# Optimization experiments

Measured on AMD Instinct MI355X. Metric: run time of the kernel, lower is better.

## Reference

```python
import jax, jax.numpy as jnp
import numpy as np
import math

N_HEAD = 16

def _rope_cos_sin(T, head_dim):
    # thetas[i] = 10000 ** (-2*(i-1)/dim) for i = 1..dim/2  ->  exponent -2*j/dim, j=0..dim/2-1
    j = jnp.arange(head_dim // 2, dtype=jnp.float32)
    theta = jnp.power(10000.0, -2.0 * j / head_dim)          # [d/2]
    t = jnp.arange(T, dtype=jnp.float32)                      # [T]
    ang = t[:, None] * theta[None, :]                         # [T, d/2]
    return jnp.cos(ang), jnp.sin(ang)

def _apply_rope(u, cos, sin):
    # u: [B,H,T,d]; interleaved complex rotation over pairs (u[...,2i], u[...,2i+1])
    B, H, T, d = u.shape
    u = u.reshape(B, H, T, d // 2, 2)
    u0, u1 = u[..., 0], u[..., 1]
    r0 = u0 * cos - u1 * sin
    r1 = u0 * sin + u1 * cos
    return jnp.stack([r0, r1], axis=-1).reshape(B, H, T, d)

def setup_inputs() -> dict:
    key = jax.random.key(0)
    ks = jax.random.split(key, 9)
    C = 1024
    s = 1.0 / math.sqrt(C)
    return {
        "x": jax.random.normal(ks[0], (4, 2048, C), dtype=jnp.float32),
        "wq": jax.random.normal(ks[1], (C, C), dtype=jnp.float32) * s,
        "bq": jax.random.normal(ks[2], (C,), dtype=jnp.float32) * s,
        "wk": jax.random.normal(ks[3], (C, C), dtype=jnp.float32) * s,
        "bk": jax.random.normal(ks[4], (C,), dtype=jnp.float32) * s,
        "wv": jax.random.normal(ks[5], (C, C), dtype=jnp.float32) * s,
        "bv": jax.random.normal(ks[6], (C,), dtype=jnp.float32) * s,
        "wp": jax.random.normal(ks[7], (C, C), dtype=jnp.float32) * s,
        "bp": jax.random.normal(ks[8], (C,), dtype=jnp.float32) * s,
    }

def reference(x, wq, bq, wk, bk, wv, bv, wp, bp):
    B, T, C = x.shape
    H = N_HEAD
    d = C // H
    def proj(w, b):
        # nn.Linear: x @ w.T + b, then split heads -> [B,H,T,d]
        return (jnp.einsum('btc,oc->bto', x, w) + b).reshape(B, T, H, d).transpose(0, 2, 1, 3)
    q, k, v = proj(wq, bq), proj(wk, bk), proj(wv, bv)
    cos, sin = _rope_cos_sin(T, d)
    q = _apply_rope(q, cos, sin)
    k = _apply_rope(k, cos, sin)
    att = jnp.einsum('bhqd,bhkd->bhqk', q, k) * (1.0 / math.sqrt(d))  # [B,H,T,T]
    causal = jnp.tril(jnp.ones((T, T), dtype=bool))
    att = jnp.where(causal, att, jnp.finfo(att.dtype).min)
    att = jax.nn.softmax(att, axis=-1)
    y = jnp.einsum('bhqk,bhkd->bhqd', att, v)                         # [B,H,T,d]
    y = y.transpose(0, 2, 1, 3).reshape(B, T, C)
    return jnp.einsum('btc,oc->bto', y, wp) + bp
```

## Files before the change

### kernel.cpp

```cpp
#include <hip/hip_runtime.h>

typedef __attribute__((ext_vector_type(8))) __bf16 bf16x8;
typedef __attribute__((ext_vector_type(4))) float f32x4;
typedef __attribute__((ext_vector_type(16))) float f32x16;
typedef unsigned short u16;

#define TSEQ   2048
#define NB     4
#define NHEAD  16
#define HDIM   64
#define CMODEL 1024
#define MTOK   (NB*TSEQ)

__device__ __forceinline__ u16 f2bf(float x){
  unsigned u = __float_as_uint(x);
  u += 0x7fffu + ((u >> 16) & 1u);
  return (u16)(u >> 16);
}

__device__ __forceinline__ unsigned cvtpk(float lo, float hi){
  unsigned r;
  asm("v_cvt_pk_bf16_f32 %0, %1, %2" : "=v"(r) : "v"(lo), "v"(hi));
  return r;
}
__device__ __forceinline__ void plswap(unsigned &a, unsigned &b){
  asm volatile("v_permlane32_swap_b32 %0, %1" : "+v"(a), "+v"(b));
}

__device__ __forceinline__ void async16(const void* g, const u16* lds_base){
  __builtin_amdgcn_global_load_lds(
      (const __attribute__((address_space(1))) unsigned*)(uintptr_t)g,
      (__attribute__((address_space(3))) unsigned*)(unsigned)(uintptr_t)lds_base,
      16, 0, 0);
}

__global__ void cast_bf16_kernel(const float* __restrict__ src, u16* __restrict__ dst, int n4){
  int i = blockIdx.x * blockDim.x + threadIdx.x;
  int stride = gridDim.x * blockDim.x;
  for (; i < n4; i += stride){
    float4 v = ((const float4*)src)[i];
    ((ushort4*)dst)[i] = make_ushort4(f2bf(v.x), f2bf(v.y), f2bf(v.z), f2bf(v.w));
  }
}

__global__ void cast4_bf16_kernel(const float* __restrict__ s0, const float* __restrict__ s1,
                                  const float* __restrict__ s2, const float* __restrict__ s3,
                                  u16* __restrict__ d0, u16* __restrict__ d1,
                                  u16* __restrict__ d2, u16* __restrict__ d3, int n4){
  int which = blockIdx.y;
  const float* s = (which==0)?s0:(which==1)?s1:(which==2)?s2:s3;
  u16* d        = (which==0)?d0:(which==1)?d1:(which==2)?d2:d3;
  int i = blockIdx.x * blockDim.x + threadIdx.x;
  int stride = gridDim.x * blockDim.x;
  for (; i < n4; i += stride){
    float4 v = ((const float4*)s)[i];
    ((ushort4*)d)[i] = make_ushort4(f2bf(v.x), f2bf(v.y), f2bf(v.z), f2bf(v.w));
  }
}

__global__ void rope_table_kernel(float2* __restrict__ rope){
  int i = blockIdx.x * blockDim.x + threadIdx.x;
  if (i >= TSEQ * (HDIM/2)) return;
  int t = i >> 5, j = i & 31;
  float theta = exp2f(-(float)j * (13.287712379549449f / 32.f));
  float ang = (float)t * theta;
  rope[i] = make_float2(cosf(ang), sinf(ang));
}

#define AREG 8192
#define BREG 16384

__device__ __forceinline__ void gemm_tb3_mainloop(
    const u16* __restrict__ A, const u16* __restrict__ B,
    int m0, int n0, u16* sAb, u16* sBb, f32x4 acc[4][4])
{
  const int tid = threadIdx.x;
  const int lane = tid & 63, w = tid >> 6;
  const int ln = lane & 15, g = lane >> 4;
  const int wm = w >> 2, wn = w & 3;

  const f32x4 zero = {0.f, 0.f, 0.f, 0.f};
#pragma unroll
  for (int i = 0; i < 4; ++i)
#pragma unroll
    for (int nt = 0; nt < 4; ++nt) acc[i][nt] = zero;

  const int cA0 = tid,       rA0 = cA0 >> 3;
  const int cA1 = 512 + tid, rA1 = cA1 >> 3;
  const u16* aS0 = A + (size_t)(m0 + rA0)*CMODEL + (((cA0 & 7) ^ (rA0 & 7)) << 3);
  const u16* aS1 = A + (size_t)(m0 + rA1)*CMODEL + (((cA1 & 7) ^ (rA1 & 7)) << 3);
  const unsigned dA0 = (unsigned)cA0 * 8, dA1 = (unsigned)cA1 * 8;
  const u16* bS[4]; unsigned dB[4];
#pragma unroll
  for (int j = 0; j < 4; ++j){
    int c = j*512 + tid, r = c >> 3;
    bS[j] = B + (size_t)(n0 + r)*CMODEL + (((c & 7) ^ (r & 7)) << 3);
    dB[j] = (unsigned)c * 8;
  }

  unsigned aoff[4][2], boff[4][2];
#pragma unroll
  for (int i = 0; i < 4; ++i){
    int r = wm*64 + i*16 + ln;
#pragma unroll
    for (int kk = 0; kk < 2; ++kk)
      aoff[i][kk] = (unsigned)(r*8 + ((kk*4 + g) ^ (r & 7))) * 8;
  }
#pragma unroll
  for (int nt = 0; nt < 4; ++nt){
    int r = wn*64 + nt*16 + ln;
#pragma unroll
    for (int kk = 0; kk < 2; ++kk)
      boff[nt][kk] = (unsigned)(r*8 + ((kk*4 + g) ^ (r & 7))) * 8;
  }

  async16(aS0,       sAb + dA0);
  async16(aS1,       sAb + dA1);
  async16(bS[0],     sBb + dB[0]);
  async16(bS[1],     sBb + dB[1]);
  async16(bS[2],     sBb + dB[2]);
  async16(bS[3],     sBb + dB[3]);
  async16(aS0 + 64,  sAb + AREG + dA0);
  async16(aS1 + 64,  sAb + AREG + dA1);
  async16(bS[0] + 64, sBb + BREG + dB[0]);
  async16(bS[1] + 64, sBb + BREG + dB[1]);
  async16(bS[2] + 64, sBb + BREG + dB[2]);
  async16(bS[3] + 64, sBb + BREG + dB[3]);
  asm volatile("s_waitcnt vmcnt(6)" ::: "memory");
  asm volatile("s_barrier" ::: "memory");

#pragma unroll 1
  for (int kt = 0; kt < 16; ++kt){
    const int cb = kt % 3;
    const int nb = (kt + 2) % 3;
    const u16* Ab = sAb + cb*AREG;
    const u16* Bb = sBb + cb*BREG;
    u16* An = sAb + nb*AREG;
    u16* Bn = sBb + nb*BREG;
    const unsigned ko = (unsigned)(kt + 2) * 64u;
    const bool st = (kt < 14);

    bf16x8 a0, a1, a2, a3, b0, b1, b2, b3;

    a0 = *(const bf16x8*)&Ab[aoff[0][0]];
    a1 = *(const bf16x8*)&Ab[aoff[1][0]];
    b0 = *(const bf16x8*)&Bb[boff[0][0]];
    b1 = *(const bf16x8*)&Bb[boff[1][0]];
    b2 = *(const bf16x8*)&Bb[boff[2][0]];
    b3 = *(const bf16x8*)&Bb[boff[3][0]];
    if (st){ async16(aS0 + ko, An + dA0); async16(aS1 + ko, An + dA1); }
    asm volatile("s_barrier" ::: "memory");
    __builtin_amdgcn_s_setprio(1);
    acc[0][0] = __builtin_amdgcn_mfma_f32_16x16x32_bf16(a0, b0, acc[0][0], 0,0,0);
    acc[0][1] = __builtin_amdgcn_mfma_f32_16x16x32_bf16(a0, b1, acc[0][1], 0,0,0);
    acc[0][2] = __builtin_amdgcn_mfma_f32_16x16x32_bf16(a0, b2, acc[0][2], 0,0,0);
    acc[0][3] = __builtin_amdgcn_mfma_f32_16x16x32_bf16(a0, b3, acc[0][3], 0,0,0);
    acc[1][0] = __builtin_amdgcn_mfma_f32_16x16x32_bf16(a1, b0, acc[1][0], 0,0,0);
    acc[1][1] = __builtin_amdgcn_mfma_f32_16x16x32_bf16(a1, b1, acc[1][1], 0,0,0);
    acc[1][2] = __builtin_amdgcn_mfma_f32_16x16x32_bf16(a1, b2, acc[1][2], 0,0,0);
    acc[1][3] = __builtin_amdgcn_mfma_f32_16x16x32_bf16(a1, b3, acc[1][3], 0,0,0);
    __builtin_amdgcn_s_setprio(0);
    asm volatile("s_barrier" ::: "memory");

    a2 = *(const bf16x8*)&Ab[aoff[2][0]];
    a3 = *(const bf16x8*)&Ab[aoff[3][0]];
    if (st){ async16(bS[0] + ko, Bn + dB[0]); async16(bS[1] + ko, Bn + dB[1]); }
    asm volatile("s_barrier" ::: "memory");
    __builtin_amdgcn_s_setprio(1);
    acc[2][0] = __builtin_amdgcn_mfma_f32_16x16x32_bf16(a2, b0, acc[2][0], 0,0,0);
    acc[2][1] = __builtin_amdgcn_mfma_f32_16x16x32_bf16(a2, b1, acc[2][1], 0,0,0);
    acc[2][2] = __builtin_amdgcn_mfma_f32_16x16x32_bf16(a2, b2, acc[2][2], 0,0,0);
    acc[2][3] = __builtin_amdgcn_mfma_f32_16x16x32_bf16(a2, b3, acc[2][3], 0,0,0);
    acc[3][0] = __builtin_amdgcn_mfma_f32_16x16x32_bf16(a3, b0, acc[3][0], 0,0,0);
    acc[3][1] = __builtin_amdgcn_mfma_f32_16x16x32_bf16(a3, b1, acc[3][1], 0,0,0);
    acc[3][2] = __builtin_amdgcn_mfma_f32_16x16x32_bf16(a3, b2, acc[3][2], 0,0,0);
    acc[3][3] = __builtin_amdgcn_mfma_f32_16x16x32_bf16(a3, b3, acc[3][3], 0,0,0);
    __builtin_amdgcn_s_setprio(0);
    asm volatile("s_barrier" ::: "memory");

    a0 = *(const bf16x8*)&Ab[aoff[0][1]];
    a1 = *(const bf16x8*)&Ab[aoff[1][1]];
    b0 = *(const bf16x8*)&Bb[boff[0][1]];
    b1 = *(const bf16x8*)&Bb[boff[1][1]];
    b2 = *(const bf16x8*)&Bb[boff[2][1]];
    b3 = *(const bf16x8*)&Bb[boff[3][1]];
    if (st) async16(bS[2] + ko, Bn + dB[2]);
    asm volatile("s_barrier" ::: "memory");
    __builtin_amdgcn_s_setprio(1);
    acc[0][0] = __builtin_amdgcn_mfma_f32_16x16x32_bf16(a0, b0, acc[0][0], 0,0,0);
    acc[0][1] = __builtin_amdgcn_mfma_f32_16x16x32_bf16(a0, b1, acc[0][1], 0,0,0);
    acc[0][2] = __builtin_amdgcn_mfma_f32_16x16x32_bf16(a0, b2, acc[0][2], 0,0,0);
    acc[0][3] = __builtin_amdgcn_mfma_f32_16x16x32_bf16(a0, b3, acc[0][3], 0,0,0);
    acc[1][0] = __builtin_amdgcn_mfma_f32_16x16x32_bf16(a1, b0, acc[1][0], 0,0,0);
    acc[1][1] = __builtin_amdgcn_mfma_f32_16x16x32_bf16(a1, b1, acc[1][1], 0,0,0);
    acc[1][2] = __builtin_amdgcn_mfma_f32_16x16x32_bf16(a1, b2, acc[1][2], 0,0,0);
    acc[1][3] = __builtin_amdgcn_mfma_f32_16x16x32_bf16(a1, b3, acc[1][3], 0,0,0);
    __builtin_amdgcn_s_setprio(0);
    asm volatile("s_barrier" ::: "memory");

    a2 = *(const bf16x8*)&Ab[aoff[2][1]];
    a3 = *(const bf16x8*)&Ab[aoff[3][1]];
    if (st) async16(bS[3] + ko, Bn + dB[3]);
    asm volatile("s_barrier" ::: "memory");
    __builtin_amdgcn_s_setprio(1);
    acc[2][0] = __builtin_amdgcn_mfma_f32_16x16x32_bf16(a2, b0, acc[2][0], 0,0,0);
    acc[2][1] = __builtin_amdgcn_mfma_f32_16x16x32_bf16(a2, b1, acc[2][1], 0,0,0);
    acc[2][2] = __builtin_amdgcn_mfma_f32_16x16x32_bf16(a2, b2, acc[2][2], 0,0,0);
    acc[2][3] = __builtin_amdgcn_mfma_f32_16x16x32_bf16(a2, b3, acc[2][3], 0,0,0);
    acc[3][0] = __builtin_amdgcn_mfma_f32_16x16x32_bf16(a3, b0, acc[3][0], 0,0,0);
    acc[3][1] = __builtin_amdgcn_mfma_f32_16x16x32_bf16(a3, b1, acc[3][1], 0,0,0);
    acc[3][2] = __builtin_amdgcn_mfma_f32_16x16x32_bf16(a3, b2, acc[3][2], 0,0,0);
    acc[3][3] = __builtin_amdgcn_mfma_f32_16x16x32_bf16(a3, b3, acc[3][3], 0,0,0);
    __builtin_amdgcn_s_setprio(0);
    if (st) asm volatile("s_waitcnt vmcnt(6)" ::: "memory");
    else    asm volatile("s_waitcnt vmcnt(0)" ::: "memory");
    asm volatile("s_barrier" ::: "memory");
  }
}

#define SCQ 0.18033688011112042f

__global__ __launch_bounds__(512, 1) void gemm_qkv_kernel(
    const u16* __restrict__ xb,
    const u16* __restrict__ wqb, const u16* __restrict__ wkb, const u16* __restrict__ wvb,
    const float* __restrict__ bq, const float* __restrict__ bk, const float* __restrict__ bv,
    const float2* __restrict__ rope,
    u16* __restrict__ Qh, u16* __restrict__ Kh, u16* __restrict__ Vt)
{
  __shared__ u16 sA[3*AREG];
  __shared__ u16 sB[3*BREG];
  const int z = blockIdx.z;
  const u16*  W    = (z == 0) ? wqb : (z == 1) ? wkb : wvb;
  const float* bias = (z == 0) ? bq  : (z == 1) ? bk  : bv;
  const int m0 = blockIdx.y * 128, n0 = blockIdx.x * 256;

  f32x4 acc[4][4];
  gemm_tb3_mainloop(xb, W, m0, n0, sA, sB, acc);

  const int tid = threadIdx.x, w = tid >> 6, lane = tid & 63;
  const int ln = lane & 15, g = lane >> 4;
  const int wm = w >> 2, wn = w & 3;

#pragma unroll
  for (int mt = 0; mt < 4; ++mt){
#pragma unroll
    for (int nt = 0; nt < 4; ++nt){
      int o  = n0 + wn*64 + nt*16 + ln;
      float bb = bias[o];
      int h  = o >> 6;
      int dd = o & 63;
      if (z < 2){
        int j = dd >> 1;
        u16* dst = (z == 0) ? Qh : Kh;
        float qs = (z == 0) ? SCQ : 1.0f;
#pragma unroll
        for (int rr = 0; rr < 4; ++rr){
          int t  = m0 + wm*64 + mt*16 + g*4 + rr;
          int b  = t >> 11, tt = t & (TSEQ-1);
          float v  = acc[mt][nt][rr] + bb;
          float pv = __shfl_xor(v, 1);
          float2 cs = rope[tt*32 + j];
          float out = ((o & 1) == 0) ? (v*cs.x - pv*cs.y) : (pv*cs.y + v*cs.x);
          dst[(size_t)((b*NHEAD + h)*TSEQ + tt)*HDIM + dd] = f2bf(out * qs);
        }
      } else {
        int t0 = m0 + wm*64 + mt*16 + g*4;
        int b  = t0 >> 11, tt0 = t0 & (TSEQ-1);
        u16 pk[4];
#pragma unroll
        for (int rr = 0; rr < 4; ++rr) pk[rr] = f2bf(acc[mt][nt][rr] + bb);
        *(ushort4*)&Vt[(size_t)((b*NHEAD + h)*HDIM + dd)*TSEQ + tt0] =
            make_ushort4(pk[0], pk[1], pk[2], pk[3]);
      }
    }
  }
}

__global__ __launch_bounds__(128) void attn_kernel(
    const u16* __restrict__ Qh, const u16* __restrict__ Kh,
    const u16* __restrict__ Vt, u16* __restrict__ yb)
{
  __shared__ u16 sK[2][64*64];
  __shared__ u16 sV[2][64*64];

  const int tid = threadIdx.x, w = tid >> 6, lane = tid & 63;
  const int ln = lane & 31, hi = lane >> 5;

  const int bid = blockIdx.x;
  const int t   = 31 - (bid >> 6);
  const int bh  = (bid & 7) * 8 + ((bid >> 3) & 7);
  const int b   = bh >> 4, h = bh & (NHEAD-1);

  const u16* Qbase = Qh + (size_t)bh * TSEQ * HDIM;
  const u16* Kbase = Kh + (size_t)bh * TSEQ * HDIM;
  const u16* Vbase = Vt + (size_t)bh * HDIM * TSEQ;

  const int r0 = t*64 + w*32;

  const int swz = ln & 7;
  const f32x16 zero16 = {0,0,0,0,0,0,0,0,0,0,0,0,0,0,0,0};

  const u16* kp[4]; const u16* vp[4]; unsigned dstc[4];
#pragma unroll
  for (int i = 0; i < 4; ++i){
    int c = i*128 + tid, r = c >> 3, pc = c & 7;
    kp[i]   = Kbase + (size_t)r*HDIM + ((pc ^ (r&7))<<3);
    vp[i]   = Vbase + (size_t)r*TSEQ + ((pc ^ (r&7))<<3);
    dstc[i] = (unsigned)(i*128 + w*64)*8;
  }

  unsigned offd[4];
#pragma unroll
  for (int d = 0; d < 4; ++d) offd[d] = ((unsigned)((2*d + hi) ^ swz)) * 8;
  const unsigned rowl = (unsigned)ln * 64;
  const unsigned rowh = rowl + 32*64;

  bf16x8 qf[4];
#pragma unroll
  for (int ds = 0; ds < 4; ++ds)
    qf[ds] = *(const bf16x8*)&Qbase[(size_t)(r0 + ln)*HDIM + ds*16 + hi*8];

  f32x16 yacc0 = zero16, yacc1 = zero16;
  float m2 = -1e30f, lp = 0.f;

  int buf = 0;
#pragma unroll
  for (int i = 0; i < 4; ++i){
    async16(kp[i], sK[0] + dstc[i]);
    async16(vp[i], sV[0] + dstc[i]);
  }

#pragma unroll 1
  for (int jt = 0; jt <= t; ++jt){
    __syncthreads();
    if (jt < t){
      const size_t ko = (size_t)(jt+1) * (64*HDIM);
      const size_t vo = (size_t)(jt+1) * 64;
      u16* sKb = sK[buf^1]; u16* sVb = sV[buf^1];
#pragma unroll
      for (int i = 0; i < 4; ++i){
        async16(kp[i] + ko, sKb + dstc[i]);
        async16(vp[i] + vo, sVb + dstc[i]);
      }
    }

    const u16* sKb = sK[buf];
    const u16* sVb = sV[buf];
    const bool full1 = (jt < t) || w;

    f32x16 p0 = zero16, p1 = zero16;
    __builtin_amdgcn_s_setprio(1);
#pragma unroll
    for (int ds = 0; ds < 4; ++ds){
      bf16x8 k0 = *(const bf16x8*)&sKb[rowl + offd[ds]];
      p0 = __builtin_amdgcn_mfma_f32_32x32x16_bf16(k0, qf[ds], p0, 0, 0, 0);
    }
    if (full1){
#pragma unroll
      for (int ds = 0; ds < 4; ++ds){
        bf16x8 k1 = *(const bf16x8*)&sKb[rowh + offd[ds]];
        p1 = __builtin_amdgcn_mfma_f32_32x32x16_bf16(k1, qf[ds], p1, 0, 0, 0);
      }
    }
    __builtin_amdgcn_s_setprio(0);

    if (jt == t){
#pragma unroll
      for (int r = 0; r < 16; ++r){
        int k0r = (r&3) + 8*(r>>2) + 4*hi;
        bool cut = k0r > ln;
        if (!w){ if (cut) p0[r] = -1e30f; }
        else   { if (cut) p1[r] = -1e30f; }
      }
    }

    float lm = p0[0];
#pragma unroll
    for (int r = 1; r < 16; ++r) lm = fmaxf(lm, p0[r]);
    if (full1){
#pragma unroll
      for (int r = 0; r < 16; ++r) lm = fmaxf(lm, p1[r]);
    }

    if (__any(lm - m2 > 8.0f)){
      float lmp = __shfl_xor(lm, 32);
      float mn  = fmaxf(m2, fmaxf(lm, lmp));
      float scl = exp2f(m2 - mn);
      m2 = mn;
      lp *= scl;
#pragma unroll
      for (int r = 0; r < 16; ++r){
        float sr = __shfl(scl, (r&3) + 8*(r>>2) + 4*hi);
        yacc0[r] *= sr; yacc1[r] *= sr;
      }
    }

    float ts = 0.f;
#pragma unroll
    for (int r = 0; r < 16; ++r){ p0[r] = exp2f(p0[r] - m2); ts += p0[r]; }
    if (full1){
#pragma unroll
      for (int r = 0; r < 16; ++r){ p1[r] = exp2f(p1[r] - m2); ts += p1[r]; }
    }
    lp += ts;

    bf16x8 pa[4];
    {
      union { unsigned u[4]; bf16x8 v; } f0, f1;
      unsigned A0 = cvtpk(p0[0], p0[1]),  B0 = cvtpk(p0[2], p0[3]);
      unsigned A1 = cvtpk(p0[4], p0[5]),  B1 = cvtpk(p0[6], p0[7]);
      plswap(A0, A1); plswap(B0, B1);
      f0.u[0]=A0; f0.u[1]=B0; f0.u[2]=A1; f0.u[3]=B1;  pa[0]=f0.v;
      unsigned A2 = cvtpk(p0[8], p0[9]),  B2 = cvtpk(p0[10], p0[11]);
      unsigned A3 = cvtpk(p0[12], p0[13]),B3 = cvtpk(p0[14], p0[15]);
      plswap(A2, A3); plswap(B2, B3);
      f1.u[0]=A2; f1.u[1]=B2; f1.u[2]=A3; f1.u[3]=B3;  pa[1]=f1.v;
    }
    if (full1){
      union { unsigned u[4]; bf16x8 v; } f2, f3;
      unsigned A4 = cvtpk(p1[0], p1[1]),  B4 = cvtpk(p1[2], p1[3]);
      unsigned A5 = cvtpk(p1[4], p1[5]),  B5 = cvtpk(p1[6], p1[7]);
      plswap(A4, A5); plswap(B4, B5);
      f2.u[0]=A4; f2.u[1]=B4; f2.u[2]=A5; f2.u[3]=B5;  pa[2]=f2.v;
      unsigned A6 = cvtpk(p1[8], p1[9]),  B6 = cvtpk(p1[10], p1[11]);
      unsigned A7 = cvtpk(p1[12], p1[13]),B7 = cvtpk(p1[14], p1[15]);
      plswap(A6, A7); plswap(B6, B7);
      f3.u[0]=A6; f3.u[1]=B6; f3.u[2]=A7; f3.u[3]=B7;  pa[3]=f3.v;
    }

    __builtin_amdgcn_s_setprio(1);
#pragma unroll
    for (int st = 0; st < 2; ++st){
      bf16x8 v0 = *(const bf16x8*)&sVb[rowl + offd[st]];
      bf16x8 v1 = *(const bf16x8*)&sVb[rowh + offd[st]];
      yacc0 = __builtin_amdgcn_mfma_f32_32x32x16_bf16(pa[st], v0, yacc0, 0, 0, 0);
      yacc1 = __builtin_amdgcn_mfma_f32_32x32x16_bf16(pa[st], v1, yacc1, 0, 0, 0);
    }
    if (full1){
#pragma unroll
      for (int st = 2; st < 4; ++st){
        bf16x8 v0 = *(const bf16x8*)&sVb[rowl + offd[st]];
        bf16x8 v1 = *(const bf16x8*)&sVb[rowh + offd[st]];
        yacc0 = __builtin_amdgcn_mfma_f32_32x32x16_bf16(pa[st], v0, yacc0, 0, 0, 0);
        yacc1 = __builtin_amdgcn_mfma_f32_32x32x16_bf16(pa[st], v1, yacc1, 0, 0, 0);
      }
    }
    __builtin_amdgcn_s_setprio(0);

    buf ^= 1;
  }

  float lpf = lp + __shfl_xor(lp, 32);
  float inv = 1.0f / lpf;
#pragma unroll
  for (int r = 0; r < 16; ++r){
    int q = (r&3) + 8*(r>>2) + 4*hi;
    float ir = __shfl(inv, q);
    int tt = r0 + q;
    size_t rowoff = (size_t)(b*TSEQ + tt)*CMODEL + h*HDIM;
    yb[rowoff + ln]      = f2bf(yacc0[r] * ir);
    yb[rowoff + 32 + ln] = f2bf(yacc1[r] * ir);
  }
}

__global__ __launch_bounds__(512, 1) void gemm_proj_kernel(
    const u16* __restrict__ yb, const u16* __restrict__ wpb,
    const float* __restrict__ bp, float* __restrict__ out)
{
  __shared__ u16 sA[3*AREG];
  __shared__ u16 sB[3*BREG];
  const int m0 = blockIdx.y * 128, n0 = blockIdx.x * 256;
  f32x4 acc[4][4];
  gemm_tb3_mainloop(yb, wpb, m0, n0, sA, sB, acc);

  const int tid = threadIdx.x, w = tid >> 6, lane = tid & 63;
  const int ln = lane & 15, g = lane >> 4;
  const int wm = w >> 2, wn = w & 3;
#pragma unroll
  for (int mt = 0; mt < 4; ++mt)
#pragma unroll
    for (int nt = 0; nt < 4; ++nt){
      int o = n0 + wn*64 + nt*16 + ln;
      float bb = bp[o];
#pragma unroll
      for (int rr = 0; rr < 4; ++rr){
        int t = m0 + wm*64 + mt*16 + g*4 + rr;
        out[(size_t)t*CMODEL + o] = acc[mt][nt][rr] + bb;
      }
    }
}

extern "C" void kernel_launch(void* const* d_in, const int* in_sizes, int n_in,
                              void* d_out, int out_size, void* d_ws, size_t ws_size,
                              hipStream_t stream)
{
  const float* x  = (const float*)d_in[0];
  const float* wq = (const float*)d_in[1];
  const float* bq = (const float*)d_in[2];
  const float* wk = (const float*)d_in[3];
  const float* bk = (const float*)d_in[4];
  const float* wv = (const float*)d_in[5];
  const float* bv = (const float*)d_in[6];
  const float* wp = (const float*)d_in[7];
  const float* bp = (const float*)d_in[8];

  char* ws = (char*)d_ws;
  u16*    xb   = (u16*)   (ws + 0);
  u16*    wqb  = (u16*)   (ws + 16777216);
  u16*    wkb  = (u16*)   (ws + 18874368);
  u16*    wvb  = (u16*)   (ws + 20971520);
  u16*    wpb  = (u16*)   (ws + 23068672);
  float2* rope = (float2*)(ws + 25165824);
  u16*    Qh   = (u16*)   (ws + 25690112);
  u16*    Kh   = (u16*)   (ws + 42467328);
  u16*    Vt   = (u16*)   (ws + 59244544);
  u16*    yb   = (u16*)   (ws + 76021760);

  cast_bf16_kernel<<<2048, 256, 0, stream>>>(x,  xb,  MTOK*CMODEL/4);
  cast4_bf16_kernel<<<dim3(256, 4), 256, 0, stream>>>(wq, wk, wv, wp, wqb, wkb, wvb, wpb,
                                                      CMODEL*CMODEL/4);
  rope_table_kernel<<<(TSEQ*(HDIM/2) + 255)/256, 256, 0, stream>>>(rope);

  gemm_qkv_kernel<<<dim3(CMODEL/256, MTOK/128, 3), 512, 0, stream>>>(
      xb, wqb, wkb, wvb, bq, bk, bv, rope, Qh, Kh, Vt);

  attn_kernel<<<dim3(2048), 128, 0, stream>>>(Qh, Kh, Vt, yb);

  gemm_proj_kernel<<<dim3(CMODEL/256, MTOK/128), 512, 0, stream>>>(yb, wpb, bp, (float*)d_out);
}
```

Before: 214.2 us.

## Shrink attention KV tile to 32 rows with per-warp causal cutoff

The attention kernel now streams K/V in 32-key tiles instead of 64-key tiles, halving shared memory per buffer and changing the swizzle layout for the V tile. Each warp only computes tiles up to its own diagonal (jtw), so the masked half-tile and the per-iteration full1 branching are gone. In exchange the loop runs twice as many iterations, each with its own barrier, async copy issue and softmax max/rescale check, and the MFMA work per sync shrinks.

Result: no change. 213.5 us (-0.3%).

```diff
diff --git a/kernel.cpp b/kernel.cpp
--- a/kernel.cpp
+++ b/kernel.cpp
@@ -280,8 +280,8 @@
     const u16* __restrict__ Qh, const u16* __restrict__ Kh,
     const u16* __restrict__ Vt, u16* __restrict__ yb)
 {
-  __shared__ u16 sK[2][64*64];
-  __shared__ u16 sV[2][64*64];
+  __shared__ u16 sK[2][32*64];
+  __shared__ u16 sV[2][64*32];
 
   const int tid = threadIdx.x, w = tid >> 6, lane = tid & 63;
   const int ln = lane & 31, hi = lane >> 5;
@@ -295,25 +295,34 @@
   const u16* Kbase = Kh + (size_t)bh * TSEQ * HDIM;
   const u16* Vbase = Vt + (size_t)bh * HDIM * TSEQ;
 
-  const int r0 = t*64 + w*32;
-
-  const int swz = ln & 7;
+  const int r0  = t*64 + w*32;
+  const int jtw = 2*t + w;
+  const int jtb = 2*t + 1;
+
   const f32x16 zero16 = {0,0,0,0,0,0,0,0,0,0,0,0,0,0,0,0};
 
-  const u16* kp[4]; const u16* vp[4]; unsigned dstc[4];
-#pragma unroll
-  for (int i = 0; i < 4; ++i){
-    int c = i*128 + tid, r = c >> 3, pc = c & 7;
-    kp[i]   = Kbase + (size_t)r*HDIM + ((pc ^ (r&7))<<3);
-    vp[i]   = Vbase + (size_t)r*TSEQ + ((pc ^ (r&7))<<3);
-    dstc[i] = (unsigned)(i*128 + w*64)*8;
-  }
-
-  unsigned offd[4];
-#pragma unroll
-  for (int d = 0; d < 4; ++d) offd[d] = ((unsigned)((2*d + hi) ^ swz)) * 8;
-  const unsigned rowl = (unsigned)ln * 64;
-  const unsigned rowh = rowl + 32*64;
+  const u16* kp[2]; const u16* vp[2]; unsigned kd[2];
+#pragma unroll
+  for (int i = 0; i < 2; ++i){
+    int c = i*128 + tid;
+    int kr = c >> 3, ks = c & 7;
+    kp[i] = Kbase + (size_t)kr*HDIM + ((ks ^ (kr&7))<<3);
+    int vr = c >> 2, vs = c & 3;
+    vp[i] = Vbase + (size_t)vr*TSEQ + ((vs ^ (vr&3))<<3);
+    kd[i] = (unsigned)c * 8;
+  }
+
+  unsigned koff[4];
+#pragma unroll
+  for (int ds = 0; ds < 4; ++ds)
+    koff[ds] = (unsigned)(ln*8 + ((2*ds + hi) ^ (ln & 7))) * 8;
+  unsigned voff0[2], voff1[2];
+#pragma unroll
+  for (int st = 0; st < 2; ++st){
+    unsigned ch = (unsigned)((2*st + hi) ^ (ln & 3)) * 8;
+    voff0[st] = (unsigned)ln*32 + ch;
+    voff1[st] = (unsigned)(32+ln)*32 + ch;
+  }
 
   bf16x8 qf[4];
 #pragma unroll
@@ -325,128 +334,91 @@
 
   int buf = 0;
 #pragma unroll
-  for (int i = 0; i < 4; ++i){
-    async16(kp[i], sK[0] + dstc[i]);
-    async16(vp[i], sV[0] + dstc[i]);
+  for (int i = 0; i < 2; ++i){
+    async16(kp[i], sK[0] + kd[i]);
+    async16(vp[i], sV[0] + kd[i]);
   }
 
 #pragma unroll 1
-  for (int jt = 0; jt <= t; ++jt){
+  for (int jt = 0; jt <= jtb; ++jt){
     __syncthreads();
-    if (jt < t){
-      const size_t ko = (size_t)(jt+1) * (64*HDIM);
-      const size_t vo = (size_t)(jt+1) * 64;
+    if (jt < jtb){
+      const size_t ko = (size_t)(jt+1) * (32*HDIM);
+      const size_t vo = (size_t)(jt+1) * 32;
       u16* sKb = sK[buf^1]; u16* sVb = sV[buf^1];
 #pragma unroll
-      for (int i = 0; i < 4; ++i){
-        async16(kp[i] + ko, sKb + dstc[i]);
-        async16(vp[i] + vo, sVb + dstc[i]);
+      for (int i = 0; i < 2; ++i){
+        async16(kp[i] + ko, sKb + kd[i]);
+        async16(vp[i] + vo, sVb + kd[i]);
       }
     }
 
-    const u16* sKb = sK[buf];
-    const u16* sVb = sV[buf];
-    const bool full1 = (jt < t) || w;
-
-    f32x16 p0 = zero16, p1 = zero16;
-    __builtin_amdgcn_s_setprio(1);
-#pragma unroll
-    for (int ds = 0; ds < 4; ++ds){
-      bf16x8 k0 = *(const bf16x8*)&sKb[rowl + offd[ds]];
-      p0 = __builtin_amdgcn_mfma_f32_32x32x16_bf16(k0, qf[ds], p0, 0, 0, 0);
-    }
-    if (full1){
+    if (jt <= jtw){
+      const u16* sKb = sK[buf];
+      const u16* sVb = sV[buf];
+
+      f32x16 p0 = zero16;
+      __builtin_amdgcn_s_setprio(1);
 #pragma unroll
       for (int ds = 0; ds < 4; ++ds){
-        bf16x8 k1 = *(const bf16x8*)&sKb[rowh + offd[ds]];
-        p1 = __builtin_amdgcn_mfma_f32_32x32x16_bf16(k1, qf[ds], p1, 0, 0, 0);
-      }
-    }
-    __builtin_amdgcn_s_setprio(0);
-
-    if (jt == t){
-#pragma unroll
-      for (int r = 0; r < 16; ++r){
-        int k0r = (r&3) + 8*(r>>2) + 4*hi;
-        bool cut = k0r > ln;
-        if (!w){ if (cut) p0[r] = -1e30f; }
-        else   { if (cut) p1[r] = -1e30f; }
-      }
-    }
-
-    float lm = p0[0];
-#pragma unroll
-    for (int r = 1; r < 16; ++r) lm = fmaxf(lm, p0[r]);
-    if (full1){
-#pragma unroll
-      for (int r = 0; r < 16; ++r) lm = fmaxf(lm, p1[r]);
-    }
-
-    if (__any(lm - m2 > 8.0f)){
-      float lmp = __shfl_xor(lm, 32);
-      float mn  = fmaxf(m2, fmaxf(lm, lmp));
-      float scl = exp2f(m2 - mn);
-      m2 = mn;
-      lp *= scl;
-#pragma unroll
-      for (int r = 0; r < 16; ++r){
-        float sr = __shfl(scl, (r&3) + 8*(r>>2) + 4*hi);
-        yacc0[r] *= sr; yacc1[r] *= sr;
-      }
-    }
-
-    float ts = 0.f;
-#pragma unroll
-    for (int r = 0; r < 16; ++r){ p0[r] = exp2f(p0[r] - m2); ts += p0[r]; }
-    if (full1){
-#pragma unroll
-      for (int r = 0; r < 16; ++r){ p1[r] = exp2f(p1[r] - m2); ts += p1[r]; }
-    }
-    lp += ts;
-
-    bf16x8 pa[4];
-    {
-      union { unsigned u[4]; bf16x8 v; } f0, f1;
-      unsigned A0 = cvtpk(p0[0], p0[1]),  B0 = cvtpk(p0[2], p0[3]);
-      unsigned A1 = cvtpk(p0[4], p0[5]),  B1 = cvtpk(p0[6], p0[7]);
-      plswap(A0, A1); plswap(B0, B1);
-      f0.u[0]=A0; f0.u[1]=B0; f0.u[2]=A1; f0.u[3]=B1;  pa[0]=f0.v;
-      unsigned A2 = cvtpk(p0[8], p0[9]),  B2 = cvtpk(p0[10], p0[11]);
-      unsigned A3 = cvtpk(p0[12], p0[13]),B3 = cvtpk(p0[14], p0[15]);
-      plswap(A2, A3); plswap(B2, B3);
-      f1.u[0]=A2; f1.u[1]=B2; f1.u[2]=A3; f1.u[3]=B3;  pa[1]=f1.v;
-    }
-    if (full1){
-      union { unsigned u[4]; bf16x8 v; } f2, f3;
-      unsigned A4 = cvtpk(p1[0], p1[1]),  B4 = cvtpk(p1[2], p1[3]);
-      unsigned A5 = cvtpk(p1[4], p1[5]),  B5 = cvtpk(p1[6], p1[7]);
-      plswap(A4, A5); plswap(B4, B5);
-      f2.u[0]=A4; f2.u[1]=B4; f2.u[2]=A5; f2.u[3]=B5;  pa[2]=f2.v;
-      unsigned A6 = cvtpk(p1[8], p1[9]),  B6 = cvtpk(p1[10], p1[11]);
-      unsigned A7 = cvtpk(p1[12], p1[13]),B7 = cvtpk(p1[14], p1[15]);
-      plswap(A6, A7); plswap(B6, B7);
-      f3.u[0]=A6; f3.u[1]=B6; f3.u[2]=A7; f3.u[3]=B7;  pa[3]=f3.v;
-    }
-
-    __builtin_amdgcn_s_setprio(1);
-#pragma unroll
-    for (int st = 0; st < 2; ++st){
-      bf16x8 v0 = *(const bf16x8*)&sVb[rowl + offd[st]];
-      bf16x8 v1 = *(const bf16x8*)&sVb[rowh + offd[st]];
-      yacc0 = __builtin_amdgcn_mfma_f32_32x32x16_bf16(pa[st], v0, yacc0, 0, 0, 0);
-      yacc1 = __builtin_amdgcn_mfma_f32_32x32x16_bf16(pa[st], v1, yacc1, 0, 0, 0);
-    }
-    if (full1){
-#pragma unroll
-      for (int st = 2; st < 4; ++st){
-        bf16x8 v0 = *(const bf16x8*)&sVb[rowl + offd[st]];
-        bf16x8 v1 = *(const bf16x8*)&sVb[rowh + offd[st]];
+        bf16x8 k0 = *(const bf16x8*)&sKb[koff[ds]];
+        p0 = __builtin_amdgcn_mfma_f32_32x32x16_bf16(k0, qf[ds], p0, 0, 0, 0);
+      }
+      __builtin_amdgcn_s_setprio(0);
+
+      if (jt == jtw){
+#pragma unroll
+        for (int r = 0; r < 16; ++r){
+          int k0r = (r&3) + 8*(r>>2) + 4*hi;
+          if (k0r > ln) p0[r] = -1e30f;
+        }
+      }
+
+      float lm = p0[0];
+#pragma unroll
+      for (int r = 1; r < 16; ++r) lm = fmaxf(lm, p0[r]);
+
+      if (__any(lm - m2 > 8.0f)){
+        float lmp = __shfl_xor(lm, 32);
+        float mn  = fmaxf(m2, fmaxf(lm, lmp));
+        float scl = exp2f(m2 - mn);
+        m2 = mn;
+        lp *= scl;
+#pragma unroll
+        for (int r = 0; r < 16; ++r){
+          float sr = __shfl(scl, (r&3) + 8*(r>>2) + 4*hi);
+          yacc0[r] *= sr; yacc1[r] *= sr;
+        }
+      }
+
+      float ts = 0.f;
+#pragma unroll
+      for (int r = 0; r < 16; ++r){ p0[r] = exp2f(p0[r] - m2); ts += p0[r]; }
+      lp += ts;
+
+      bf16x8 pa[2];
+      {
+        union { unsigned u[4]; bf16x8 v; } f0, f1;
+        unsigned A0 = cvtpk(p0[0], p0[1]),  B0 = cvtpk(p0[2], p0[3]);
+        unsigned A1 = cvtpk(p0[4], p0[5]),  B1 = cvtpk(p0[6], p0[7]);
+        plswap(A0, A1); plswap(B0, B1);
+        f0.u[0]=A0; f0.u[1]=B0; f0.u[2]=A1; f0.u[3]=B1;  pa[0]=f0.v;
+        unsigned A2 = cvtpk(p0[8], p0[9]),  B2 = cvtpk(p0[10], p0[11]);
+        unsigned A3 = cvtpk(p0[12], p0[13]),B3 = cvtpk(p0[14], p0[15]);
+        plswap(A2, A3); plswap(B2, B3);
+        f1.u[0]=A2; f1.u[1]=B2; f1.u[2]=A3; f1.u[3]=B3;  pa[1]=f1.v;
+      }
+
+      __builtin_amdgcn_s_setprio(1);
+#pragma unroll
+      for (int st = 0; st < 2; ++st){
+        bf16x8 v0 = *(const bf16x8*)&sVb[voff0[st]];
+        bf16x8 v1 = *(const bf16x8*)&sVb[voff1[st]];
         yacc0 = __builtin_amdgcn_mfma_f32_32x32x16_bf16(pa[st], v0, yacc0, 0, 0, 0);
         yacc1 = __builtin_amdgcn_mfma_f32_32x32x16_bf16(pa[st], v1, yacc1, 0, 0, 0);
       }
+      __builtin_amdgcn_s_setprio(0);
     }
-    __builtin_amdgcn_s_setprio(0);
-
     buf ^= 1;
   }
 
```

## Restructure attention into 8-wave blocks with triple-buffered KV and paired tiles

Applied to the files above, without the earlier changes.

The attention kernel now uses 512-thread blocks, each handling a 256-row query strip per pass for one batch-head, so one K/V tile load in shared memory is shared by eight waves instead of two. Each block does two strips (s and 7-s) to balance causal work, and the grid shrinks to 256 blocks, one per CU. The shared-memory ring grows to three stages, with explicit vmcnt waits and raw barriers. The cost is fewer blocks and less occupancy to hide latency, plus idle waves on the diagonal tiles of each strip.

Result: faster. 199.8 us (-6.7%).

```diff
diff --git a/kernel.cpp b/kernel.cpp
--- a/kernel.cpp
+++ b/kernel.cpp
@@ -276,190 +276,196 @@
   }
 }
 
-__global__ __launch_bounds__(128) void attn_kernel(
+__global__ __launch_bounds__(512, 1) void attn_kernel(
     const u16* __restrict__ Qh, const u16* __restrict__ Kh,
     const u16* __restrict__ Vt, u16* __restrict__ yb)
 {
-  __shared__ u16 sK[2][64*64];
-  __shared__ u16 sV[2][64*64];
+  __shared__ u16 sK[3][64*64];
+  __shared__ u16 sV[3][64*64];
 
   const int tid = threadIdx.x, w = tid >> 6, lane = tid & 63;
   const int ln = lane & 31, hi = lane >> 5;
 
   const int bid = blockIdx.x;
-  const int t   = 31 - (bid >> 6);
-  const int bh  = (bid & 7) * 8 + ((bid >> 3) & 7);
+  const int bh  = bid >> 2;
+  const int pr  = bid & 3;
   const int b   = bh >> 4, h = bh & (NHEAD-1);
 
   const u16* Qbase = Qh + (size_t)bh * TSEQ * HDIM;
   const u16* Kbase = Kh + (size_t)bh * TSEQ * HDIM;
   const u16* Vbase = Vt + (size_t)bh * HDIM * TSEQ;
 
-  const int r0 = t*64 + w*32;
+  const int cr = tid >> 3, cs = tid & 7;
+  const u16* kp = Kbase + (size_t)cr*HDIM + ((cs ^ (cr&7))<<3);
+  const u16* vp = Vbase + (size_t)cr*TSEQ + ((cs ^ (cr&7))<<3);
+  const unsigned dstw = (unsigned)(w*64)*8;
 
   const int swz = ln & 7;
-  const f32x16 zero16 = {0,0,0,0,0,0,0,0,0,0,0,0,0,0,0,0};
-
-  const u16* kp[4]; const u16* vp[4]; unsigned dstc[4];
-#pragma unroll
-  for (int i = 0; i < 4; ++i){
-    int c = i*128 + tid, r = c >> 3, pc = c & 7;
-    kp[i]   = Kbase + (size_t)r*HDIM + ((pc ^ (r&7))<<3);
-    vp[i]   = Vbase + (size_t)r*TSEQ + ((pc ^ (r&7))<<3);
-    dstc[i] = (unsigned)(i*128 + w*64)*8;
-  }
-
   unsigned offd[4];
 #pragma unroll
   for (int d = 0; d < 4; ++d) offd[d] = ((unsigned)((2*d + hi) ^ swz)) * 8;
   const unsigned rowl = (unsigned)ln * 64;
   const unsigned rowh = rowl + 32*64;
 
-  bf16x8 qf[4];
-#pragma unroll
-  for (int ds = 0; ds < 4; ++ds)
-    qf[ds] = *(const bf16x8*)&Qbase[(size_t)(r0 + ln)*HDIM + ds*16 + hi*8];
-
-  f32x16 yacc0 = zero16, yacc1 = zero16;
-  float m2 = -1e30f, lp = 0.f;
-
-  int buf = 0;
-#pragma unroll
-  for (int i = 0; i < 4; ++i){
-    async16(kp[i], sK[0] + dstc[i]);
-    async16(vp[i], sV[0] + dstc[i]);
-  }
+  const f32x16 zero16 = {0,0,0,0,0,0,0,0,0,0,0,0,0,0,0,0};
+  const int wodd = w & 1;
 
 #pragma unroll 1
-  for (int jt = 0; jt <= t; ++jt){
-    __syncthreads();
-    if (jt < t){
-      const size_t ko = (size_t)(jt+1) * (64*HDIM);
-      const size_t vo = (size_t)(jt+1) * 64;
-      u16* sKb = sK[buf^1]; u16* sVb = sV[buf^1];
-#pragma unroll
-      for (int i = 0; i < 4; ++i){
-        async16(kp[i] + ko, sKb + dstc[i]);
-        async16(vp[i] + vo, sVb + dstc[i]);
+  for (int ss = 0; ss < 2; ++ss){
+    const int s   = ss ? pr : (7 - pr);
+    const int r0  = s*256 + w*32;
+    const int jtb = 4*s + 3;
+    const int jtw = 4*s + (w >> 1);
+    const size_t kvoff = 0;
+
+    bf16x8 qf[4];
+#pragma unroll
+    for (int ds = 0; ds < 4; ++ds)
+      qf[ds] = *(const bf16x8*)&Qbase[(size_t)(r0 + ln)*HDIM + ds*16 + hi*8];
+
+    f32x16 yacc0 = zero16, yacc1 = zero16;
+    float m2 = -1e30f, lp = 0.f;
+
+    async16(kp,                       sK[0] + dstw);
+    async16(vp,                       sV[0] + dstw);
+    async16(kp + (size_t)64*HDIM,     sK[1] + dstw);
+    async16(vp + 64,                  sV[1] + dstw);
+    asm volatile("s_waitcnt vmcnt(2)" ::: "memory");
+    asm volatile("s_barrier" ::: "memory");
+
+#pragma unroll 1
+    for (int jt = 0; jt <= jtb; ++jt){
+      const bool st2 = (jt + 2 <= jtb);
+      if (st2){
+        const int nb = (jt + 2) % 3;
+        async16(kp + (size_t)(jt+2)*64*HDIM, sK[nb] + dstw);
+        async16(vp + (size_t)(jt+2)*64,      sV[nb] + dstw);
       }
+
+      if (jt <= jtw){
+        const int cb = jt % 3;
+        const u16* sKb = sK[cb];
+        const u16* sVb = sV[cb];
+        const bool full1 = (jt < jtw) || wodd;
+
+        f32x16 p0 = zero16, p1 = zero16;
+        __builtin_amdgcn_s_setprio(1);
+#pragma unroll
+        for (int ds = 0; ds < 4; ++ds){
+          bf16x8 k0 = *(const bf16x8*)&sKb[rowl + offd[ds]];
+          p0 = __builtin_amdgcn_mfma_f32_32x32x16_bf16(k0, qf[ds], p0, 0, 0, 0);
+        }
+        if (full1){
+#pragma unroll
+          for (int ds = 0; ds < 4; ++ds){
+            bf16x8 k1 = *(const bf16x8*)&sKb[rowh + offd[ds]];
+            p1 = __builtin_amdgcn_mfma_f32_32x32x16_bf16(k1, qf[ds], p1, 0, 0, 0);
+          }
+        }
+        __builtin_amdgcn_s_setprio(0);
+
+        if (jt == jtw){
+#pragma unroll
+          for (int r = 0; r < 16; ++r){
+            int k0r = (r&3) + 8*(r>>2) + 4*hi;
+            bool cut = k0r > ln;
+            if (!wodd){ if (cut) p0[r] = -1e30f; }
+            else      { if (cut) p1[r] = -1e30f; }
+          }
+        }
+
+        float lm = p0[0];
+#pragma unroll
+        for (int r = 1; r < 16; ++r) lm = fmaxf(lm, p0[r]);
+        if (full1){
+#pragma unroll
+          for (int r = 0; r < 16; ++r) lm = fmaxf(lm, p1[r]);
+        }
+
+        if (__any(lm - m2 > 8.0f)){
+          float lmp = __shfl_xor(lm, 32);
+          float mn  = fmaxf(m2, fmaxf(lm, lmp));
+          float scl = exp2f(m2 - mn);
+          m2 = mn;
+          lp *= scl;
+#pragma unroll
+          for (int r = 0; r < 16; ++r){
+            float sr = __shfl(scl, (r&3) + 8*(r>>2) + 4*hi);
+            yacc0[r] *= sr; yacc1[r] *= sr;
+          }
+        }
+
+        float ts = 0.f;
+#pragma unroll
+        for (int r = 0; r < 16; ++r){ p0[r] = exp2f(p0[r] - m2); ts += p0[r]; }
+        if (full1){
+#pragma unroll
+          for (int r = 0; r < 16; ++r){ p1[r] = exp2f(p1[r] - m2); ts += p1[r]; }
+        }
+        lp += ts;
+
+        bf16x8 pa[4];
+        {
+          union { unsigned u[4]; bf16x8 v; } f0, f1;
+          unsigned A0 = cvtpk(p0[0], p0[1]),  B0 = cvtpk(p0[2], p0[3]);
+          unsigned A1 = cvtpk(p0[4], p0[5]),  B1 = cvtpk(p0[6], p0[7]);
+          plswap(A0, A1); plswap(B0, B1);
+          f0.u[0]=A0; f0.u[1]=B0; f0.u[2]=A1; f0.u[3]=B1;  pa[0]=f0.v;
+          unsigned A2 = cvtpk(p0[8], p0[9]),  B2 = cvtpk(p0[10], p0[11]);
+          unsigned A3 = cvtpk(p0[12], p0[13]),B3 = cvtpk(p0[14], p0[15]);
+          plswap(A2, A3); plswap(B2, B3);
+          f1.u[0]=A2; f1.u[1]=B2; f1.u[2]=A3; f1.u[3]=B3;  pa[1]=f1.v;
+        }
+        if (full1){
+          union { unsigned u[4]; bf16x8 v; } f2, f3;
+          unsigned A4 = cvtpk(p1[0], p1[1]),  B4 = cvtpk(p1[2], p1[3]);
+          unsigned A5 = cvtpk(p1[4], p1[5]),  B5 = cvtpk(p1[6], p1[7]);
+          plswap(A4, A5); plswap(B4, B5);
+          f2.u[0]=A4; f2.u[1]=B4; f2.u[2]=A5; f2.u[3]=B5;  pa[2]=f2.v;
+          unsigned A6 = cvtpk(p1[8], p1[9]),  B6 = cvtpk(p1[10], p1[11]);
+          unsigned A7 = cvtpk(p1[12], p1[13]),B7 = cvtpk(p1[14], p1[15]);
+          plswap(A6, A7); plswap(B6, B7);
+          f3.u[0]=A6; f3.u[1]=B6; f3.u[2]=A7; f3.u[3]=B7;  pa[3]=f3.v;
+        }
+
+        __builtin_amdgcn_s_setprio(1);
+#pragma unroll
+        for (int st = 0; st < 2; ++st){
+          bf16x8 v0 = *(const bf16x8*)&sVb[rowl + offd[st]];
+          bf16x8 v1 = *(const bf16x8*)&sVb[rowh + offd[st]];
+          yacc0 = __builtin_amdgcn_mfma_f32_32x32x16_bf16(pa[st], v0, yacc0, 0, 0, 0);
+          yacc1 = __builtin_amdgcn_mfma_f32_32x32x16_bf16(pa[st], v1, yacc1, 0, 0, 0);
+        }
+        if (full1){
+#pragma unroll
+          for (int st = 2; st < 4; ++st){
+            bf16x8 v0 = *(const bf16x8*)&sVb[rowl + offd[st]];
+            bf16x8 v1 = *(const bf16x8*)&sVb[rowh + offd[st]];
+            yacc0 = __builtin_amdgcn_mfma_f32_32x32x16_bf16(pa[st], v0, yacc0, 0, 0, 0);
+            yacc1 = __builtin_amdgcn_mfma_f32_32x32x16_bf16(pa[st], v1, yacc1, 0, 0, 0);
+          }
+        }
+        __builtin_amdgcn_s_setprio(0);
+      }
+
+      if (st2) asm volatile("s_waitcnt vmcnt(2)" ::: "memory");
+      else     asm volatile("s_waitcnt vmcnt(0)" ::: "memory");
+      asm volatile("s_barrier" ::: "memory");
+      (void)kvoff;
     }
 
-    const u16* sKb = sK[buf];
-    const u16* sVb = sV[buf];
-    const bool full1 = (jt < t) || w;
-
-    f32x16 p0 = zero16, p1 = zero16;
-    __builtin_amdgcn_s_setprio(1);
-#pragma unroll
-    for (int ds = 0; ds < 4; ++ds){
-      bf16x8 k0 = *(const bf16x8*)&sKb[rowl + offd[ds]];
-      p0 = __builtin_amdgcn_mfma_f32_32x32x16_bf16(k0, qf[ds], p0, 0, 0, 0);
+    float lpf = lp + __shfl_xor(lp, 32);
+    float inv = 1.0f / lpf;
+#pragma unroll
+    for (int r = 0; r < 16; ++r){
+      int q = (r&3) + 8*(r>>2) + 4*hi;
+      float ir = __shfl(inv, q);
+      int tt = r0 + q;
+      size_t rowoff = (size_t)(b*TSEQ + tt)*CMODEL + h*HDIM;
+      yb[rowoff + ln]      = f2bf(yacc0[r] * ir);
+      yb[rowoff + 32 + ln] = f2bf(yacc1[r] * ir);
     }
-    if (full1){
-#pragma unroll
-      for (int ds = 0; ds < 4; ++ds){
-        bf16x8 k1 = *(const bf16x8*)&sKb[rowh + offd[ds]];
-        p1 = __builtin_amdgcn_mfma_f32_32x32x16_bf16(k1, qf[ds], p1, 0, 0, 0);
-      }
-    }
-    __builtin_amdgcn_s_setprio(0);
-
-    if (jt == t){
-#pragma unroll
-      for (int r = 0; r < 16; ++r){
-        int k0r = (r&3) + 8*(r>>2) + 4*hi;
-        bool cut = k0r > ln;
-        if (!w){ if (cut) p0[r] = -1e30f; }
-        else   { if (cut) p1[r] = -1e30f; }
-      }
-    }
-
-    float lm = p0[0];
-#pragma unroll
-    for (int r = 1; r < 16; ++r) lm = fmaxf(lm, p0[r]);
-    if (full1){
-#pragma unroll
-      for (int r = 0; r < 16; ++r) lm = fmaxf(lm, p1[r]);
-    }
-
-    if (__any(lm - m2 > 8.0f)){
-      float lmp = __shfl_xor(lm, 32);
-      float mn  = fmaxf(m2, fmaxf(lm, lmp));
-      float scl = exp2f(m2 - mn);
-      m2 = mn;
-      lp *= scl;
-#pragma unroll
-      for (int r = 0; r < 16; ++r){
-        float sr = __shfl(scl, (r&3) + 8*(r>>2) + 4*hi);
-        yacc0[r] *= sr; yacc1[r] *= sr;
-      }
-    }
-
-    float ts = 0.f;
-#pragma unroll
-    for (int r = 0; r < 16; ++r){ p0[r] = exp2f(p0[r] - m2); ts += p0[r]; }
-    if (full1){
-#pragma unroll
-      for (int r = 0; r < 16; ++r){ p1[r] = exp2f(p1[r] - m2); ts += p1[r]; }
-    }
-    lp += ts;
-
-    bf16x8 pa[4];
-    {
-      union { unsigned u[4]; bf16x8 v; } f0, f1;
-      unsigned A0 = cvtpk(p0[0], p0[1]),  B0 = cvtpk(p0[2], p0[3]);
-      unsigned A1 = cvtpk(p0[4], p0[5]),  B1 = cvtpk(p0[6], p0[7]);
-      plswap(A0, A1); plswap(B0, B1);
-      f0.u[0]=A0; f0.u[1]=B0; f0.u[2]=A1; f0.u[3]=B1;  pa[0]=f0.v;
-      unsigned A2 = cvtpk(p0[8], p0[9]),  B2 = cvtpk(p0[10], p0[11]);
-      unsigned A3 = cvtpk(p0[12], p0[13]),B3 = cvtpk(p0[14], p0[15]);
-      plswap(A2, A3); plswap(B2, B3);
-      f1.u[0]=A2; f1.u[1]=B2; f1.u[2]=A3; f1.u[3]=B3;  pa[1]=f1.v;
-    }
-    if (full1){
-      union { unsigned u[4]; bf16x8 v; } f2, f3;
-      unsigned A4 = cvtpk(p1[0], p1[1]),  B4 = cvtpk(p1[2], p1[3]);
-      unsigned A5 = cvtpk(p1[4], p1[5]),  B5 = cvtpk(p1[6], p1[7]);
-      plswap(A4, A5); plswap(B4, B5);
-      f2.u[0]=A4; f2.u[1]=B4; f2.u[2]=A5; f2.u[3]=B5;  pa[2]=f2.v;
-      unsigned A6 = cvtpk(p1[8], p1[9]),  B6 = cvtpk(p1[10], p1[11]);
-      unsigned A7 = cvtpk(p1[12], p1[13]),B7 = cvtpk(p1[14], p1[15]);
-      plswap(A6, A7); plswap(B6, B7);
-      f3.u[0]=A6; f3.u[1]=B6; f3.u[2]=A7; f3.u[3]=B7;  pa[3]=f3.v;
-    }
-
-    __builtin_amdgcn_s_setprio(1);
-#pragma unroll
-    for (int st = 0; st < 2; ++st){
-      bf16x8 v0 = *(const bf16x8*)&sVb[rowl + offd[st]];
-      bf16x8 v1 = *(const bf16x8*)&sVb[rowh + offd[st]];
-      yacc0 = __builtin_amdgcn_mfma_f32_32x32x16_bf16(pa[st], v0, yacc0, 0, 0, 0);
-      yacc1 = __builtin_amdgcn_mfma_f32_32x32x16_bf16(pa[st], v1, yacc1, 0, 0, 0);
-    }
-    if (full1){
-#pragma unroll
-      for (int st = 2; st < 4; ++st){
-        bf16x8 v0 = *(const bf16x8*)&sVb[rowl + offd[st]];
-        bf16x8 v1 = *(const bf16x8*)&sVb[rowh + offd[st]];
-        yacc0 = __builtin_amdgcn_mfma_f32_32x32x16_bf16(pa[st], v0, yacc0, 0, 0, 0);
-        yacc1 = __builtin_amdgcn_mfma_f32_32x32x16_bf16(pa[st], v1, yacc1, 0, 0, 0);
-      }
-    }
-    __builtin_amdgcn_s_setprio(0);
-
-    buf ^= 1;
-  }
-
-  float lpf = lp + __shfl_xor(lp, 32);
-  float inv = 1.0f / lpf;
-#pragma unroll
-  for (int r = 0; r < 16; ++r){
-    int q = (r&3) + 8*(r>>2) + 4*hi;
-    float ir = __shfl(inv, q);
-    int tt = r0 + q;
-    size_t rowoff = (size_t)(b*TSEQ + tt)*CMODEL + h*HDIM;
-    yb[rowoff + ln]      = f2bf(yacc0[r] * ir);
-    yb[rowoff + 32 + ln] = f2bf(yacc1[r] * ir);
+    asm volatile("s_barrier" ::: "memory");
   }
 }
 
@@ -524,7 +530,7 @@
   gemm_qkv_kernel<<<dim3(CMODEL/256, MTOK/128, 3), 512, 0, stream>>>(
       xb, wqb, wkb, wvb, bq, bk, bv, rope, Qh, Kh, Vt);
 
-  attn_kernel<<<dim3(2048), 128, 0, stream>>>(Qh, Kh, Vt, yb);
+  attn_kernel<<<dim3(256), 512, 0, stream>>>(Qh, Kh, Vt, yb);
 
   gemm_proj_kernel<<<dim3(CMODEL/256, MTOK/128), 512, 0, stream>>>(yb, wpb, bp, (float*)d_out);
 }
```
